# Kernel optimization log

Measured on AMD Instinct MI355X. Metric: run time of the kernel, lower is better.

## Reference

```python
import jax, jax.numpy as jnp
import numpy as np

B, L, M, H = 4096, 512, 17, 17  # batch, seq_len, num_features, latent_dim


def setup_inputs() -> dict:
    key = jax.random.key(0)
    ks = jax.random.split(key, 5)
    s = 1.0 / np.sqrt(H)  # torch nn.LSTM init scale
    x = jax.random.normal(ks[0], (B, L, M), dtype=jnp.float32)
    W_ih = jax.random.uniform(ks[1], (4 * H, M), dtype=jnp.float32, minval=-s, maxval=s)
    W_hh = jax.random.uniform(ks[2], (4 * H, H), dtype=jnp.float32, minval=-s, maxval=s)
    b_ih = jax.random.uniform(ks[3], (4 * H,), dtype=jnp.float32, minval=-s, maxval=s)
    b_hh = jax.random.uniform(ks[4], (4 * H,), dtype=jnp.float32, minval=-s, maxval=s)
    return {"x": x, "W_ih": W_ih, "W_hh": W_hh, "b_ih": b_ih, "b_hh": b_hh}


def _lstm(x, W_ih, W_hh, b_ih, b_hh):
    # Precompute input projections for all timesteps in one GEMM: (B,L,4H)
    xW = jnp.einsum('blm,gm->blg', x, W_ih) + b_ih + b_hh
    xW_t = jnp.swapaxes(xW, 0, 1)  # (L,B,4H) for scan over time
    W_hh_T = W_hh.T  # (H,4H)

    def step(carry, xw_t):
        h, c = carry
        gates = xw_t + h @ W_hh_T  # (B,4H)
        i, f, g, o = jnp.split(gates, 4, axis=-1)  # torch gate order: i,f,g,o
        i = jax.nn.sigmoid(i)
        f = jax.nn.sigmoid(f)
        g = jnp.tanh(g)
        o = jax.nn.sigmoid(o)
        c_new = f * c + i * g
        h_new = o * jnp.tanh(c_new)
        return (h_new, c_new), h_new

    h0 = jnp.zeros((x.shape[0], W_hh.shape[1]), dtype=x.dtype)
    c0 = jnp.zeros_like(h0)
    (h_f, c_f), hs = jax.lax.scan(step, (h0, c0), xW_t)
    out = jnp.swapaxes(hs, 0, 1)  # (B,L,H)
    return out, h_f, c_f


def reference(x, W_ih, W_hh, b_ih, b_hh):
    out, h_f, c_f = _lstm(x, W_ih, W_hh, b_ih, b_hh)
    # match torch return: out, (h,c) with leading num_layers dim, and x
    return out, (h_f[None], c_f[None]), x
```

## Files before the change

### kernel.cpp

```cpp
#include <hip/hip_runtime.h>
#include <hip/hip_bf16.h>


namespace {
constexpr int B_TOT = 4096;
constexpr int L_SEQ = 512;
constexpr int NF    = 17;
constexpr int BS    = 16;
constexpr int TPB   = 320;
constexpr int TC    = 32;
constexpr int NCHUNK = L_SEQ / TC;
constexpr int KPAD  = 24;
constexpr int F4_PER_ROW   = TC * NF / 4;
constexpr int F4_PER_CHUNK = BS * F4_PER_ROW;
constexpr int PF_MAX = (F4_PER_CHUNK + TPB - 1) / TPB;

constexpr int OUT_H = B_TOT * L_SEQ * NF;
constexpr int OUT_C = OUT_H + B_TOT * NF;
constexpr int OUT_X = OUT_C + B_TOT * NF;
}

typedef __attribute__((ext_vector_type(8))) short bf16x8;
typedef __attribute__((ext_vector_type(4))) float f32x4;

__device__ __forceinline__ unsigned short f2bf(float f) {
  union { float f; unsigned int u; } v; v.f = f;
  unsigned int r = v.u + 0x7fff + ((v.u >> 16) & 1);
  return (unsigned short)(r >> 16);
}
__device__ __forceinline__ unsigned short h2bf(float f) {
  unsigned int r;
  asm("v_cvt_pk_bf16_f32 %0, %1, %2" : "=v"(r) : "v"(f), "v"(f));
  return (unsigned short)r;
}
__device__ __forceinline__ float sigm(float x) {
  return __builtin_amdgcn_rcpf(1.f + __expf(-x));
}
__device__ __forceinline__ float tanh_fast(float x) {
  float e = __expf(2.f * x);
  return 1.f - 2.f * __builtin_amdgcn_rcpf(e + 1.f);
}

__device__ __forceinline__ void block_sync_lds() {
  asm volatile("s_waitcnt lgkmcnt(0)" ::: "memory");
  __builtin_amdgcn_s_barrier();
  asm volatile("" ::: "memory");
}

__global__ void __launch_bounds__(TPB) lstm_kernel(
    const float* __restrict__ x, const float* __restrict__ W_ih,
    const float* __restrict__ W_hh, const float* __restrict__ b_ih,
    const float* __restrict__ b_hh, float* __restrict__ out)
{
  __shared__ __align__(16) unsigned short x_s[2][TC][BS][KPAD];
  __shared__ __align__(16) unsigned short h_s[2][BS][KPAD];
  __shared__ __align__(16) unsigned short w0_s[80][32];
  __shared__ __align__(16) unsigned short w1_s[80][32];
  __shared__ __align__(16) float bias_s[80];
  __shared__ __align__(16) unsigned short zero16[8];

  const int tid  = threadIdx.x;
  const int lane = tid & 63;
  const int T    = tid >> 6;
  const int bb   = lane & 15;
  const int q    = lane >> 4;
  const int b0   = blockIdx.x * BS;

  f32x4 pf[PF_MAX];
  #pragma unroll
  for (int i = 0; i < PF_MAX; ++i) {
    int u = tid + TPB * i;
    if (u < F4_PER_CHUNK) {
      int row = u / F4_PER_ROW, off = u % F4_PER_ROW;
      pf[i] = *(const f32x4*)(x + ((b0 + row) * L_SEQ) * NF + off * 4);
    }
  }

  {
    unsigned int* p = (unsigned int*)&x_s[0][0][0][0];
    for (int u = tid; u < (int)(sizeof(x_s) / 4); u += TPB) p[u] = 0;
    unsigned int* ph = (unsigned int*)&h_s[0][0][0];
    for (int u = tid; u < (int)(sizeof(h_s) / 4); u += TPB) ph[u] = 0;
    if (tid < 4) ((unsigned int*)zero16)[tid] = 0;
  }
  for (int u = tid; u < 80 * 32; u += TPB) {
    int r = u >> 5, k = u & 31;
    unsigned short v0 = 0, v1 = 0;
    int j = -1, ty = 0;
    if (r < 64)      { j = r >> 2; ty = r & 3; }
    else if (r < 68) { j = 16;     ty = r - 64; }
    if (j >= 0 && k < NF) {
      int g = ty * NF + j;
      v0 = f2bf(W_ih[g * NF + k]);
      v1 = f2bf(W_hh[g * NF + k]);
    }
    w0_s[r][k] = v0; w1_s[r][k] = v1;
  }
  for (int u = tid; u < 80; u += TPB) {
    float bv = 0.f; int j = -1, ty = 0;
    if (u < 64)      { j = u >> 2; ty = u & 3; }
    else if (u < 68) { j = 16;     ty = u - 64; }
    if (j >= 0) { int g = ty * NF + j; bv = b_ih[g] + b_hh[g]; }
    bias_s[u] = bv;
  }
  __syncthreads();

  auto stage = [&](int cn) {
    #pragma unroll
    for (int i = 0; i < PF_MAX; ++i) {
      int u = tid + TPB * i;
      if (u < F4_PER_CHUNK) {
        int row = u / F4_PER_ROW, off = u % F4_PER_ROW;
        int gidx = ((b0 + row) * L_SEQ + cn * TC) * NF + off * 4;
        *(f32x4*)(out + OUT_X + gidx) = pf[i];
        int p = off * 4, tl = p / NF, m = p - tl * NF;
        #pragma unroll
        for (int e = 0; e < 4; ++e) {
          x_s[cn & 1][tl][row][m] = f2bf(pf[i][e]);
          if (++m == NF) { m = 0; ++tl; }
        }
      }
    }
  };
  auto prefetch = [&](int cn) {
    #pragma unroll
    for (int i = 0; i < PF_MAX; ++i) {
      int u = tid + TPB * i;
      if (u < F4_PER_CHUNK) {
        int row = u / F4_PER_ROW, off = u % F4_PER_ROW;
        pf[i] = *(const f32x4*)(x + ((b0 + row) * L_SEQ + cn * TC) * NF + off * 4);
      }
    }
  };

  stage(0);
  prefetch(1);

  const bf16x8 a0 = *(const bf16x8*)&w0_s[16 * T + bb][q * 8];
  const bf16x8 a1 = *(const bf16x8*)&w1_s[16 * T + bb][q * 8];
  const f32x4 bias4 = *(const f32x4*)&bias_s[16 * T + q * 4];

  const int j = 4 * T + q;
  const bool active = (T < 4) || (q == 0);
  const int jj = (j > 16) ? 16 : j;

  const unsigned short* const xbase0 = (q == 3) ? zero16 : &x_s[0][0][bb][q * 8];
  const unsigned short* const xbase1 = (q == 3) ? zero16 : &x_s[1][0][bb][q * 8];
  const int xstep = (q == 3) ? 0 : BS * KPAD;
  const unsigned short* const hr0 = (q == 3) ? zero16 : &h_s[0][bb][q * 8];
  const unsigned short* const hr1 = (q == 3) ? zero16 : &h_s[1][bb][q * 8];
  unsigned short* const hw0 = &h_s[1][bb][jj];
  unsigned short* const hw1 = &h_s[0][bb][jj];

  float c_st = 0.f, h_last = 0.f;
  float* outp = out + (b0 + bb) * L_SEQ * NF + jj;

  auto epilogue = [&](const f32x4& acc, unsigned short* hwp) {
    if (active) {
      float gi = sigm(acc[0]);
      float gf = sigm(acc[1]);
      float gg = tanh_fast(acc[2]);
      float go = sigm(acc[3]);
      c_st   = gf * c_st + gi * gg;
      h_last = go * tanh_fast(c_st);
      *hwp = h2bf(h_last);
      outp[0] = h_last;
      outp += NF;
    }
  };

  f32x4 accx_e{}, accx_o{};

  for (int c = 0; c < NCHUNK; ++c) {
    const unsigned short* xp = (c & 1) ? xbase1 : xbase0;
    #pragma unroll
    for (int tt = 0; tt < TC; tt += 2) {
      block_sync_lds();
      if (tt == 0) {
        bf16x8 bx = *(const bf16x8*)xp;
        accx_e = __builtin_amdgcn_mfma_f32_16x16x32_bf16(a0, bx, bias4, 0, 0, 0);
      }
      {
        bf16x8 bh = *(const bf16x8*)hr0;
        f32x4 acc = __builtin_amdgcn_mfma_f32_16x16x32_bf16(a1, bh, accx_e, 0, 0, 0);
        bf16x8 bxo = *(const bf16x8*)(xp + xstep);
        accx_o = __builtin_amdgcn_mfma_f32_16x16x32_bf16(a0, bxo, bias4, 0, 0, 0);
        epilogue(acc, hw0);
      }
      block_sync_lds();
      {
        bf16x8 bh = *(const bf16x8*)hr1;
        f32x4 acc = __builtin_amdgcn_mfma_f32_16x16x32_bf16(a1, bh, accx_o, 0, 0, 0);
        if (tt + 2 < TC) {
          bf16x8 bxe = *(const bf16x8*)(xp + 2 * xstep);
          accx_e = __builtin_amdgcn_mfma_f32_16x16x32_bf16(a0, bxe, bias4, 0, 0, 0);
        }
        epilogue(acc, hw1);
      }
      xp += 2 * xstep;
    }
    if (c + 1 < NCHUNK) {
      stage(c + 1);
      if (c + 2 < NCHUNK) prefetch(c + 2);
    }
  }

  if (active) {
    out[OUT_H + (b0 + bb) * NF + j] = h_last;
    out[OUT_C + (b0 + bb) * NF + j] = c_st;
  }
}

extern "C" void kernel_launch(void* const* d_in, const int* in_sizes, int n_in,
                              void* d_out, int out_size, void* d_ws, size_t ws_size,
                              hipStream_t stream) {
  (void)in_sizes; (void)n_in; (void)out_size; (void)d_ws; (void)ws_size;
  const float* x    = (const float*)d_in[0];
  const float* W_ih = (const float*)d_in[1];
  const float* W_hh = (const float*)d_in[2];
  const float* b_ih = (const float*)d_in[3];
  const float* b_hh = (const float*)d_in[4];
  float* out = (float*)d_out;
  hipLaunchKernelGGL(lstm_kernel, dim3(B_TOT / BS), dim3(TPB), 0, stream,
                     x, W_ih, W_hh, b_ih, b_hh, out);
}
```

Before: 465.9 us.

## Batch input-projection MFMAs per chunk ahead of recurrence; use inline-asm stores

```diff
diff --git a/kernel.cpp b/kernel.cpp
--- a/kernel.cpp
+++ b/kernel.cpp
@@ -8,7 +8,7 @@
 constexpr int NF    = 17;
 constexpr int BS    = 16;
 constexpr int TPB   = 320;
-constexpr int TC    = 32;
+constexpr int TC    = 16;
 constexpr int NCHUNK = L_SEQ / TC;
 constexpr int KPAD  = 24;
 constexpr int F4_PER_ROW   = TC * NF / 4;
@@ -39,6 +39,13 @@
 __device__ __forceinline__ float tanh_fast(float x) {
   float e = __expf(2.f * x);
   return 1.f - 2.f * __builtin_amdgcn_rcpf(e + 1.f);
+}
+
+__device__ __forceinline__ void gstore1(float* p, float v) {
+  asm volatile("global_store_dword %0, %1, off" :: "v"(p), "v"(v));
+}
+__device__ __forceinline__ void gstore4(float* p, f32x4 v) {
+  asm volatile("global_store_dwordx4 %0, %1, off" :: "v"(p), "v"(v));
 }
 
 __device__ __forceinline__ void block_sync_lds() {
@@ -112,7 +119,7 @@
       if (u < F4_PER_CHUNK) {
         int row = u / F4_PER_ROW, off = u % F4_PER_ROW;
         int gidx = ((b0 + row) * L_SEQ + cn * TC) * NF + off * 4;
-        *(f32x4*)(out + OUT_X + gidx) = pf[i];
+        gstore4(out + OUT_X + gidx, pf[i]);
         int p = off * 4, tl = p / NF, m = p - tl * NF;
         #pragma unroll
         for (int e = 0; e < 4; ++e) {
@@ -164,41 +171,38 @@
       c_st   = gf * c_st + gi * gg;
       h_last = go * tanh_fast(c_st);
       *hwp = h2bf(h_last);
-      outp[0] = h_last;
+      gstore1(outp, h_last);
       outp += NF;
     }
   };
 
-  f32x4 accx_e{}, accx_o{};
-
   for (int c = 0; c < NCHUNK; ++c) {
-    const unsigned short* xp = (c & 1) ? xbase1 : xbase0;
+    block_sync_lds();
+
+    const unsigned short* xq = (c & 1) ? xbase1 : xbase0;
+    f32x4 hist[TC];
+    #pragma unroll
+    for (int tt = 0; tt < TC; ++tt) {
+      bf16x8 bx = *(const bf16x8*)(xq + tt * xstep);
+      hist[tt] = __builtin_amdgcn_mfma_f32_16x16x32_bf16(a0, bx, bias4, 0, 0, 0);
+    }
+
     #pragma unroll
     for (int tt = 0; tt < TC; tt += 2) {
       block_sync_lds();
-      if (tt == 0) {
-        bf16x8 bx = *(const bf16x8*)xp;
-        accx_e = __builtin_amdgcn_mfma_f32_16x16x32_bf16(a0, bx, bias4, 0, 0, 0);
-      }
       {
         bf16x8 bh = *(const bf16x8*)hr0;
-        f32x4 acc = __builtin_amdgcn_mfma_f32_16x16x32_bf16(a1, bh, accx_e, 0, 0, 0);
-        bf16x8 bxo = *(const bf16x8*)(xp + xstep);
-        accx_o = __builtin_amdgcn_mfma_f32_16x16x32_bf16(a0, bxo, bias4, 0, 0, 0);
+        f32x4 acc = __builtin_amdgcn_mfma_f32_16x16x32_bf16(a1, bh, hist[tt], 0, 0, 0);
         epilogue(acc, hw0);
       }
       block_sync_lds();
       {
         bf16x8 bh = *(const bf16x8*)hr1;
-        f32x4 acc = __builtin_amdgcn_mfma_f32_16x16x32_bf16(a1, bh, accx_o, 0, 0, 0);
-        if (tt + 2 < TC) {
-          bf16x8 bxe = *(const bf16x8*)(xp + 2 * xstep);
-          accx_e = __builtin_amdgcn_mfma_f32_16x16x32_bf16(a0, bxe, bias4, 0, 0, 0);
-        }
+        f32x4 acc = __builtin_amdgcn_mfma_f32_16x16x32_bf16(a1, bh, hist[tt + 1], 0, 0, 0);
         epilogue(acc, hw1);
       }
-      xp += 2 * xstep;
-    }
+    }
+
     if (c + 1 < NCHUNK) {
       stage(c + 1);
       if (c + 2 < NCHUNK) prefetch(c + 2);
@@ -206,8 +210,8 @@
   }
 
   if (active) {
-    out[OUT_H + (b0 + bb) * NF + j] = h_last;
-    out[OUT_C + (b0 + bb) * NF + j] = c_st;
+    gstore1(out + OUT_H + (b0 + bb) * NF + j, h_last);
+    gstore1(out + OUT_C + (b0 + bb) * NF + j, c_st);
   }
 }
 
```

Measured after the change: 454.7 us. -2.4%, faster.
